# Kernel optimization log

Measured on AMD Instinct MI355X. Metric: run time of the kernel, lower is better.

## Reference

```python
import jax, jax.numpy as jnp
import numpy as np

NUM_CLASSES = 2
CONF_THRESH = 0.05
NMS_THRESH = 0.3
NMS_TOP_K = 5000
TOP_K = 750
VAR0, VAR1 = 0.1, 0.2
NEG = -1e9  # sentinel for suppressed / below-threshold scores

NUM = 16
PRIORS = 131072


def setup_inputs() -> dict:
    key = jax.random.key(0)
    k1, k2, k3 = jax.random.split(key, 3)
    loc_data = jax.random.normal(k1, (NUM, PRIORS, 4), dtype=jnp.float32)
    conf_data = jax.random.uniform(k2, (NUM * PRIORS, NUM_CLASSES), dtype=jnp.float32)
    prior_data = jax.random.uniform(k3, (PRIORS, 4), dtype=jnp.float32)
    return {"loc_data": loc_data, "conf_data": conf_data, "prior_data": prior_data}


def decode(loc, priors):
    # loc, priors: [N, 4] (cx, cy, w, h priors); SSD box decode -> (x1, y1, x2, y2)
    xy = priors[:, :2] + loc[:, :2] * VAR0 * priors[:, 2:]
    wh = priors[:, 2:] * jnp.exp(loc[:, 2:] * VAR1)
    return jnp.concatenate([xy - wh * 0.5, xy + wh * 0.5], axis=-1)


def _area(b):
    return (b[..., 2] - b[..., 0]) * (b[..., 3] - b[..., 1])


def iou_one_to_many(box, boxes):
    # box: [4], boxes: [K, 4]
    lt = jnp.maximum(box[:2], boxes[:, :2])
    rb = jnp.minimum(box[2:], boxes[:, 2:])
    wh = jnp.clip(rb - lt, 0.0)
    inter = wh[:, 0] * wh[:, 1]
    union = _area(box) + _area(boxes) - inter
    return inter / jnp.maximum(union, 1e-12)


def nms_single(boxes, scores):
    # boxes: [P, 4], scores: [P] (one image, one class) -> [TOP_K, 5] (score, x1, y1, x2, y2)
    s = jnp.where(scores > CONF_THRESH, scores, NEG)
    top_s, top_i = jax.lax.top_k(s, NMS_TOP_K)
    top_b = boxes[top_i]  # [K, 4]
    idx_range = jnp.arange(NMS_TOP_K)

    def step(s_work, _):
        idx = jnp.argmax(s_work)
        sc = s_work[idx]
        valid = sc > NEG * 0.5
        box = top_b[idx]
        ious = iou_one_to_many(box, top_b)
        kill = (ious > NMS_THRESH) | (idx_range == idx)
        s_new = jnp.where(kill, NEG, s_work)
        row = jnp.where(valid, jnp.concatenate([sc[None], box]), jnp.zeros((5,), boxes.dtype))
        return s_new, row

    _, rows = jax.lax.scan(step, top_s, None, length=TOP_K)
    return rows  # [TOP_K, 5]


def reference(loc_data, conf_data, prior_data):
    num, P, _ = loc_data.shape
    conf = conf_data.reshape(num, P, NUM_CLASSES).transpose(0, 2, 1)  # [num, C, P]
    batch_priors = jnp.broadcast_to(prior_data, (num, P, 4)).reshape(-1, 4)
    boxes = decode(loc_data.reshape(-1, 4), batch_priors).reshape(num, P, 4)
    # NMS over non-background classes, vmapped over batch and class
    per_image = jax.vmap(nms_single, in_axes=(None, 0))          # over classes
    det = jax.vmap(per_image)(boxes, conf[:, 1:, :])             # [num, C-1, TOP_K, 5]
    bg = jnp.zeros((num, 1, TOP_K, 5), det.dtype)
    return jnp.concatenate([bg, det], axis=1)                     # [num, C, TOP_K, 5]
```

## Files before the change

### kernel.cpp

```cpp
#include <hip/hip_runtime.h>
#include <cmath>

#pragma clang fp contract(off)

typedef unsigned long long ull;

#define NPRIORS 131072
#define NIMG 16
#define KSEL 5000
#define TOPK 750
#define SORTN 8192
#define MW 80
#define NCHUNK 79
#define KSELP (NCHUNK * 64)
#define NBIN 65536

#define MID03 0.30000002682209014892578125

#define WS_PAIRS 0
#define WS_NDIAG 0
#define WS_MCNT 1048576
#define WS_BOXES 1048832
#define WS_SCORES 2328832
#define WS_MASK 2649088
#define WS_HIST (WS_MASK)
#define WS_CNT  (WS_MASK + 4194304)
#define WS_POS  (WS_MASK + 8388608)
#define WS_DIAG (WS_MASK + (size_t)NIMG * KSEL * MW * 8)

__device__ inline ull readlane64(ull t, int l) {
  unsigned lo = (unsigned)__builtin_amdgcn_readlane((int)(unsigned)t, l);
  unsigned hi = (unsigned)__builtin_amdgcn_readlane((int)(unsigned)(t >> 32), l);
  return ((ull)hi << 32) | lo;
}

__device__ inline void softBarrier() {
  asm volatile("s_waitcnt lgkmcnt(0)\n\ts_barrier" ::: "memory");
}

__global__ __launch_bounds__(256) void hist_kernel(const float* __restrict__ conf,
                                                   unsigned int* __restrict__ hist) {
  const int img = blockIdx.y;
  const float4* c4 = (const float4*)conf + (size_t)img * (NPRIORS / 2);
  unsigned int* H = hist + (size_t)img * NBIN;
  for (int q = blockIdx.x * 256 + threadIdx.x; q < NPRIORS / 2; q += 64 * 256) {
    float4 v = c4[q];
    if (v.y > 0.05f) atomicAdd(&H[(__float_as_uint(v.y) >> 12) & 0xFFFFu], 1u);
    if (v.w > 0.05f) atomicAdd(&H[(__float_as_uint(v.w) >> 12) & 0xFFFFu], 1u);
  }
}

__global__ __launch_bounds__(1024) void cutoff_kernel(const unsigned int* __restrict__ hist,
                                                      unsigned int* __restrict__ pos,
                                                      int* __restrict__ meta,
                                                      float4* __restrict__ sboxes,
                                                      float* __restrict__ sscores) {
  const int img = blockIdx.x;
  const int tid = threadIdx.x;
  const int lane = tid & 63;
  const int wv = tid >> 6;
  const unsigned int* H = hist + (size_t)img * NBIN;
  unsigned int* P = pos + (size_t)img * NBIN;
  __shared__ unsigned int csum[1024];
  __shared__ unsigned int suf[1024];
  __shared__ int s_cc;
  __shared__ unsigned int s_cut, s_mc;

  for (int g = 0; g < 64; ++g) {
    unsigned int v = H[g * 1024 + tid];
    for (int m = 1; m < 64; m <<= 1) v += __shfl_xor(v, m);
    if (lane == 0) csum[g * 16 + wv] = v;
  }
  __syncthreads();
  suf[tid] = csum[tid];
  if (tid == 0) s_cc = 0;
  __syncthreads();
  for (int off = 1; off < 1024; off <<= 1) {
    unsigned int v = (tid + off < 1024) ? suf[tid + off] : 0u;
    __syncthreads();
    suf[tid] += v;
    __syncthreads();
  }
  if (suf[tid] >= KSEL && (suf[tid] - csum[tid]) < KSEL) s_cc = tid;
  __syncthreads();
  const int cc = s_cc;
  if (tid == 0) { s_cut = (unsigned int)(cc * 64); s_mc = suf[0]; }
  __syncthreads();
  for (int b = cc * 64 + tid; b < NBIN; b += 1024) {
    int q = b >> 6;
    unsigned int acc = (q + 1 < 1024) ? suf[q + 1] : 0u;
    for (int b2 = b + 1; b2 < (q + 1) * 64; ++b2) acc += H[b2];
    P[b] = acc;
    unsigned int h = H[b];
    if (acc < KSEL && acc + h >= KSEL) { s_cut = (unsigned int)b; s_mc = acc + h; }
  }
  __syncthreads();
  if (tid == 0) {
    meta[img] = (int)min(s_mc, (unsigned int)SORTN);
    meta[16 + img] = (int)s_cut;
  }
  for (int i = tid; i < KSEL; i += 1024) {
    sboxes[(size_t)img * KSEL + i] = make_float4(0.f, 0.f, 0.f, 0.f);
    sscores[(size_t)img * KSEL + i] = -1e9f;
  }
}

__global__ __launch_bounds__(256) void scatter_kernel(const float* __restrict__ conf,
                                                      const unsigned int* __restrict__ pos,
                                                      unsigned int* __restrict__ cnt,
                                                      const int* __restrict__ meta,
                                                      ull* __restrict__ pairs) {
  const int img = blockIdx.y;
  const float4* c4 = (const float4*)conf + (size_t)img * (NPRIORS / 2);
  const unsigned int* P = pos + (size_t)img * NBIN;
  unsigned int* Cn = cnt + (size_t)img * NBIN;
  ull* mypairs = pairs + (size_t)img * SORTN;
  const unsigned int cutval = ((unsigned int)meta[16 + img]) << 12;
  for (int q = blockIdx.x * 256 + threadIdx.x; q < NPRIORS / 2; q += 64 * 256) {
    float4 v = c4[q];
#pragma unroll
    for (int h = 0; h < 2; ++h) {
      float sc = h ? v.w : v.y;
      unsigned int p = 2 * (unsigned int)q + h;
      if (sc > 0.05f) {
        unsigned int u = __float_as_uint(sc);
        if (u >= cutval) {
          unsigned int bin = (u >> 12) & 0xFFFFu;
          unsigned int slot = atomicAdd(&Cn[bin], 1u);
          unsigned int idx = P[bin] + slot;
          if (idx < SORTN)
            mypairs[idx] = ((ull)u << 32) | (ull)(0xFFFFFFFFu - p);
        }
      }
    }
  }
}

__global__ __launch_bounds__(256) void rank_decode_kernel(const ull* __restrict__ pairs,
                                                          const unsigned int* __restrict__ hist,
                                                          const unsigned int* __restrict__ pos,
                                                          const int* __restrict__ meta,
                                                          const float* __restrict__ loc,
                                                          const float* __restrict__ prior,
                                                          float4* __restrict__ sboxes,
                                                          float* __restrict__ sscores) {
#pragma clang fp contract(off)
  const int img = blockIdx.y;
  const int s = blockIdx.x * 256 + threadIdx.x;
  const int mc = meta[img];
  if (s >= mc) return;
  const ull* mypairs = pairs + (size_t)img * SORTN;
  const ull key = mypairs[s];
  const unsigned int u = (unsigned int)(key >> 32);
  const unsigned int bin = (u >> 12) & 0xFFFFu;
  const unsigned int base = pos[(size_t)img * NBIN + bin];
  const unsigned int cb = hist[(size_t)img * NBIN + bin];
  const int end = min((int)(base + cb), mc);
  int rank = 0;
  for (int j = (int)base; j < end; ++j) rank += (mypairs[j] > key);
  const int fp = (int)base + rank;
  if (fp >= KSEL) return;
  const unsigned int p = 0xFFFFFFFFu - (unsigned int)(key & 0xFFFFFFFFu);
  const float* lp = loc + ((size_t)img * NPRIORS + p) * 4;
  const float* pp = prior + (size_t)p * 4;
  float l0 = lp[0], l1 = lp[1], l2 = lp[2], l3 = lp[3];
  float px = pp[0], py = pp[1], pw = pp[2], ph = pp[3];
  float cx = px + (l0 * 0.1f) * pw;
  float cy = py + (l1 * 0.1f) * ph;
  float w = pw * (float)exp((double)(l2 * 0.2f));
  float hh = ph * (float)exp((double)(l3 * 0.2f));
  float4 box;
  box.x = cx - w * 0.5f;
  box.y = cy - hh * 0.5f;
  box.z = cx + w * 0.5f;
  box.w = cy + hh * 0.5f;
  sboxes[(size_t)img * KSEL + fp] = box;
  sscores[(size_t)img * KSEL + fp] = __uint_as_float(u);
}

__global__ __launch_bounds__(256) void mask_build_kernel(const float4* __restrict__ sboxes,
                                                         ull* __restrict__ mask,
                                                         ull* __restrict__ diag,
                                                         ull* __restrict__ ndiag) {
#pragma clang fp contract(off)
  const int jt = blockIdx.x;
  const int sp = blockIdx.y;
  const int img = blockIdx.z;
  if (jt < (sp >> 1)) return;
  const int tid = threadIdx.x;
  const int lane = tid & 63;
  const int wave = tid >> 6;
  __shared__ float4 ib[128];
  const float4* bb = sboxes + (size_t)img * KSEL;
  if (tid < 128) {
    int i = sp * 128 + tid;
    ib[tid] = (i < KSEL) ? bb[i] : make_float4(0.f, 0.f, 0.f, 0.f);
  }
  __syncthreads();
  float4 cb[4];
  float ca[4];
#pragma unroll
  for (int s = 0; s < 4; ++s) {
    int j = jt * 256 + s * 64 + lane;
    cb[s] = (j < KSEL) ? bb[j] : make_float4(0.f, 0.f, 0.f, 0.f);
    ca[s] = (cb[s].z - cb[s].x) * (cb[s].w - cb[s].y);
  }
  ull* mrow = mask + (size_t)img * KSEL * MW;
  ull* dg = diag + (size_t)img * KSELP;
  ull* ndg = ndiag + (size_t)img * KSELP;
  const int grp0 = jt * 4;
  for (int k = 0; k < 32; ++k) {
    const int rr = wave * 32 + k;
    const int strip = 2 * sp + (rr >> 6);
    const int r = rr & 63;
    const int i = sp * 128 + rr;
    const float4 pb = ib[rr];
    const float pa = (pb.z - pb.x) * (pb.w - pb.y);
    ull w[4];
#pragma unroll
    for (int s = 0; s < 4; ++s) {
      float ltx = fmaxf(pb.x, cb[s].x), lty = fmaxf(pb.y, cb[s].y);
      float rbx = fminf(pb.z, cb[s].z), rby = fminf(pb.w, cb[s].w);
      float ww = fmaxf(rbx - ltx, 0.0f), hh = fmaxf(rby - lty, 0.0f);
      float inter = ww * hh;
      float uni = fmaxf(pa + ca[s] - inter, 1e-12f);
      bool cond = ((grp0 + s) != strip) | (lane > r);
      bool kill = cond && ((double)inter > MID03 * (double)uni);
      w[s] = __ballot(kill);
    }
    if (lane == 0 && i < KSEL) {
      ull* wp = mrow + (size_t)i * MW + grp0;
      ((ulonglong2*)wp)[0] = make_ulonglong2(w[0], w[1]);
      ((ulonglong2*)wp)[1] = make_ulonglong2(w[2], w[3]);
#pragma unroll
      for (int s = 0; s < 4; ++s) {
        if (grp0 + s == strip) dg[i] = w[s];
        if (grp0 + s == strip + 1) ndg[i] = w[s];
      }
    }
  }
}

__global__ __launch_bounds__(128) void sweep_kernel(const ull* __restrict__ mask,
                                                    const ull* __restrict__ diag,
                                                    const ull* __restrict__ ndiag,
                                                    const float4* __restrict__ sboxes,
                                                    const float* __restrict__ sscores,
                                                    const int* __restrict__ meta,
                                                    float* __restrict__ out) {
  const int img = blockIdx.x;
  const int tid = threadIdx.x;
  const int lane = tid & 63;
  const bool waveA = (tid < 64);
  const int V = min(meta[img], KSEL);
  const ull* mb = mask + (size_t)img * KSEL * MW;
  const ull* dg = diag + (size_t)img * KSELP;
  const ull* ng = ndiag + (size_t)img * KSELP;
  __shared__ ull mailbox[NCHUNK + 1];
  __shared__ int pickbuf[TOPK];
  __shared__ int s_np[NCHUNK];
  __shared__ int s_start[NCHUNK];
  __shared__ int s_done;
  __shared__ int s_n;
  const int lc = min(lane, 39);

  for (int i = tid; i <= NCHUNK; i += 128) mailbox[i] = 0ULL;
  if (tid == 0) { s_done = 0; s_n = 0; }
  __syncthreads();

  if (V > 0) {
    ull dw = 0, ndw = 0, bridge = 0;
    ull rlo = 0, rhi = 0;
    int nkeep = 0;
    bool adone = false;
    if (waveA) { dw = dg[lane]; ndw = ng[lane]; }

    for (int k = 0; k < NCHUNK; ++k) {
      softBarrier();
      if (s_done) break;
      if (waveA) {
        if (!adone) {
          const int base = k * 64;
          const int nidx = min(base + 64 + lane, KSELP - 1);
          ull dwn = dg[nidx];
          ull ndwn = ng[nidx];
          ull cur = mailbox[k] | bridge;
          bridge = 0ULL;
          const int lim = V - base;
          ull validm = (lim >= 64) ? ~0ULL : ((~0ULL) >> (64 - lim));
          ull avail = (~cur) & validm;
          const int st = nkeep;
          if (lane == 0) s_start[k] = st;
          while (avail != 0ULL && nkeep < TOPK) {
            int r = __builtin_ctzll(avail);
            if (lane == 0) pickbuf[nkeep] = base + r;
            nkeep++;
            ull dr = readlane64(dw, r);
            bridge |= readlane64(ndw, r);
            avail &= ~(dr | (1ULL << r));
          }
          if (lane == 0) s_np[k] = nkeep - st;
          if (nkeep >= TOPK || base + 64 >= V) {
            if (lane == 0) { s_done = 1; s_n = (nkeep < TOPK) ? nkeep : TOPK; }
            adone = true;
          }
          dw = dwn;
          ndw = ndwn;
        }
      } else if (k >= 1) {
        const int np = s_np[k - 1];
        const int st = s_start[k - 1];
        for (int g = 0; g < np; g += 16) {
          ulonglong2 v[16];
#pragma unroll
          for (int q = 0; q < 16; ++q) {
            int t = min(g + q, np - 1);
            int row = pickbuf[st + t];
            v[q] = *(const ulonglong2*)(mb + (size_t)row * MW + 2 * lc);
          }
#pragma unroll
          for (int q = 0; q < 16; ++q) { rlo |= v[q].x; rhi |= v[q].y; }
        }
        const int w = k + 1;
        if (w < NCHUNK) {
          ull t = (w & 1) ? rhi : rlo;
          ull word = readlane64(t, w >> 1);
          if (lane == 0) mailbox[w] = word;
        }
      }
    }
  }

  __syncthreads();
  const int n = s_n;
  float* ob = out + (size_t)img * (2 * TOPK * 5) + TOPK * 5;
  for (int j = tid; j < n; j += 128) {
    int i = pickbuf[j];
    float4 b = sboxes[(size_t)img * KSEL + i];
    float sc = sscores[(size_t)img * KSEL + i];
    float* o = ob + (size_t)j * 5;
    o[0] = sc; o[1] = b.x; o[2] = b.y; o[3] = b.z; o[4] = b.w;
  }
}

extern "C" void kernel_launch(void* const* d_in, const int* in_sizes, int n_in,
                              void* d_out, int out_size, void* d_ws, size_t ws_size,
                              hipStream_t stream) {
  const float* loc = (const float*)d_in[0];
  const float* conf = (const float*)d_in[1];
  const float* prior = (const float*)d_in[2];
  float* out = (float*)d_out;

  char* ws = (char*)d_ws;
  ull* pairs = (ull*)(ws + WS_PAIRS);
  ull* ndiag = (ull*)(ws + WS_NDIAG);
  int* meta = (int*)(ws + WS_MCNT);
  float4* sboxes = (float4*)(ws + WS_BOXES);
  float* sscores = (float*)(ws + WS_SCORES);
  ull* mask = (ull*)(ws + WS_MASK);
  ull* diag = (ull*)(ws + WS_DIAG);
  unsigned int* hist = (unsigned int*)(ws + WS_HIST);
  unsigned int* cnt = (unsigned int*)(ws + WS_CNT);
  unsigned int* pos = (unsigned int*)(ws + WS_POS);

  hipMemsetAsync(d_out, 0, (size_t)out_size * sizeof(float), stream);
  hipMemsetAsync(ws + WS_HIST, 0, 2u * 4194304u, stream);

  {
    dim3 g(64, NIMG);
    hist_kernel<<<g, 256, 0, stream>>>(conf, hist);
  }
  cutoff_kernel<<<NIMG, 1024, 0, stream>>>(hist, pos, meta, sboxes, sscores);
  {
    dim3 g(64, NIMG);
    scatter_kernel<<<g, 256, 0, stream>>>(conf, pos, cnt, meta, pairs);
  }
  {
    dim3 g((SORTN + 255) / 256, NIMG);
    rank_decode_kernel<<<g, 256, 0, stream>>>(pairs, hist, pos, meta, loc, prior, sboxes, sscores);
  }
  {
    dim3 g(20, 40, NIMG);
    mask_build_kernel<<<g, 256, 0, stream>>>(sboxes, mask, diag, ndiag);
  }
  sweep_kernel<<<NIMG, 128, 0, stream>>>(mask, diag, ndiag, sboxes, sscores, meta, out);
}
```

Baseline: 534.5 us.

## Restructure NMS mask build to per-lane row bitmasks with fast IoU test

The IoU mask kernel now gives each lane one row box and loops over 256 column boxes held in shared memory. It assembles 32-bit kill words in registers instead of using one ballot per row per column group, which removes the per-row serialized lane-0 stores. The exact double-precision threshold comparison is replaced by a float FMA test with a narrow uncertainty band, falling back to double only when a wave contains a near-tie. The grid changes to 256x256 tiles, which halves the row-tile count and adds more per-thread work and register pressure.

```diff
diff --git a/kernel.cpp b/kernel.cpp
--- a/kernel.cpp
+++ b/kernel.cpp
@@ -4,6 +4,7 @@
 #pragma clang fp contract(off)
 
 typedef unsigned long long ull;
+typedef unsigned int uint;
 
 #define NPRIORS 131072
 #define NIMG 16
@@ -184,60 +185,86 @@
                                                          ull* __restrict__ ndiag) {
 #pragma clang fp contract(off)
   const int jt = blockIdx.x;
-  const int sp = blockIdx.y;
+  const int rt = blockIdx.y;
   const int img = blockIdx.z;
-  if (jt < (sp >> 1)) return;
+  if (jt < rt) return;
   const int tid = threadIdx.x;
   const int lane = tid & 63;
-  const int wave = tid >> 6;
-  __shared__ float4 ib[128];
+  const int wv = __builtin_amdgcn_readfirstlane(tid >> 6);
   const float4* bb = sboxes + (size_t)img * KSEL;
-  if (tid < 128) {
-    int i = sp * 128 + tid;
-    ib[tid] = (i < KSEL) ? bb[i] : make_float4(0.f, 0.f, 0.f, 0.f);
-  }
-  __syncthreads();
-  float4 cb[4];
-  float ca[4];
+
+  __shared__ float4 cbox[256];
+  __shared__ float carea[256];
+  {
+    int j = jt * 256 + tid;
+    float4 c = (j < KSEL) ? bb[j] : make_float4(0.f, 0.f, 0.f, 0.f);
+    cbox[tid] = c;
+    carea[tid] = (c.z - c.x) * (c.w - c.y);
+  }
+  __syncthreads();
+
+  const int R = rt * 256 + wv * 64;
+  if (R >= KSEL) return;
+  const int i = R + lane;
+  float4 pb = (i < KSEL) ? bb[i] : make_float4(0.f, 0.f, 0.f, 0.f);
+  const float pa = (pb.z - pb.x) * (pb.w - pb.y);
+
+  auto killbit = [&](int j) -> uint {
+    float4 c = cbox[j];
+    float caa = carea[j];
+    float ltx = fmaxf(pb.x, c.x), lty = fmaxf(pb.y, c.y);
+    float rbx = fminf(pb.z, c.z), rby = fminf(pb.w, c.w);
+    float ww = fmaxf(rbx - ltx, 0.0f), hh = fmaxf(rby - lty, 0.0f);
+    float inter = ww * hh;
+    float uni = fmaxf(pa + caa - inter, 1e-12f);
+    float f = fmaf(-0.3f, uni, inter);
+    float band = uni * 0x1p-20f;
+    bool kill = f > band;
+    if (__builtin_expect(__ballot(fabsf(f) <= band) != 0ULL, 0)) {
+      if (fabsf(f) <= band) kill = (double)inter > MID03 * (double)uni;
+    }
+    return kill ? 1u : 0u;
+  };
+
+  uint wl[4], wh[4];
 #pragma unroll
   for (int s = 0; s < 4; ++s) {
-    int j = jt * 256 + s * 64 + lane;
-    cb[s] = (j < KSEL) ? bb[j] : make_float4(0.f, 0.f, 0.f, 0.f);
-    ca[s] = (cb[s].z - cb[s].x) * (cb[s].w - cb[s].y);
-  }
-  ull* mrow = mask + (size_t)img * KSEL * MW;
-  ull* dg = diag + (size_t)img * KSELP;
-  ull* ndg = ndiag + (size_t)img * KSELP;
-  const int grp0 = jt * 4;
-  for (int k = 0; k < 32; ++k) {
-    const int rr = wave * 32 + k;
-    const int strip = 2 * sp + (rr >> 6);
-    const int r = rr & 63;
-    const int i = sp * 128 + rr;
-    const float4 pb = ib[rr];
-    const float pa = (pb.z - pb.x) * (pb.w - pb.y);
-    ull w[4];
-#pragma unroll
-    for (int s = 0; s < 4; ++s) {
-      float ltx = fmaxf(pb.x, cb[s].x), lty = fmaxf(pb.y, cb[s].y);
-      float rbx = fminf(pb.z, cb[s].z), rby = fminf(pb.w, cb[s].w);
-      float ww = fmaxf(rbx - ltx, 0.0f), hh = fmaxf(rby - lty, 0.0f);
-      float inter = ww * hh;
-      float uni = fmaxf(pa + ca[s] - inter, 1e-12f);
-      bool cond = ((grp0 + s) != strip) | (lane > r);
-      bool kill = cond && ((double)inter > MID03 * (double)uni);
-      w[s] = __ballot(kill);
-    }
-    if (lane == 0 && i < KSEL) {
-      ull* wp = mrow + (size_t)i * MW + grp0;
-      ((ulonglong2*)wp)[0] = make_ulonglong2(w[0], w[1]);
-      ((ulonglong2*)wp)[1] = make_ulonglong2(w[2], w[3]);
-#pragma unroll
-      for (int s = 0; s < 4; ++s) {
-        if (grp0 + s == strip) dg[i] = w[s];
-        if (grp0 + s == strip + 1) ndg[i] = w[s];
+    if (jt == rt && s < wv) { wl[s] = 0u; wh[s] = 0u; continue; }
+    uint alo = 0, ahi = 0;
+#pragma unroll 8
+    for (int b = 0; b < 32; ++b) alo |= killbit(s * 64 + b) << b;
+#pragma unroll 8
+    for (int b = 0; b < 32; ++b) ahi |= killbit(s * 64 + 32 + b) << b;
+    wl[s] = alo; wh[s] = ahi;
+  }
+
+  if (jt == rt) {
+    uint mlo, mhi;
+    if (lane < 32) { mlo = 0xFFFFFFFEu << lane; mhi = 0xFFFFFFFFu; }
+    else           { mlo = 0u; mhi = 0xFFFFFFFEu << (lane - 32); }
+    uint dl, dh;
+    if (wv == 0)      { wl[0] &= mlo; wh[0] &= mhi; dl = wl[0]; dh = wh[0]; }
+    else if (wv == 1) { wl[1] &= mlo; wh[1] &= mhi; dl = wl[1]; dh = wh[1]; }
+    else if (wv == 2) { wl[2] &= mlo; wh[2] &= mhi; dl = wl[2]; dh = wh[2]; }
+    else              { wl[3] &= mlo; wh[3] &= mhi; dl = wl[3]; dh = wh[3]; }
+    if (i < KSEL) {
+      diag[(size_t)img * KSELP + i] = ((ull)dh << 32) | dl;
+      if (wv < 3) {
+        uint nl, nh;
+        if (wv == 0)      { nl = wl[1]; nh = wh[1]; }
+        else if (wv == 1) { nl = wl[2]; nh = wh[2]; }
+        else              { nl = wl[3]; nh = wh[3]; }
+        ndiag[(size_t)img * KSELP + i] = ((ull)nh << 32) | nl;
       }
     }
+  }
+  if (jt == rt + 1 && wv == 3 && i < KSEL)
+    ndiag[(size_t)img * KSELP + i] = ((ull)wh[0] << 32) | wl[0];
+
+  if (i < KSEL) {
+    uint* wp = (uint*)(mask + (size_t)img * KSEL * MW + (size_t)i * MW) + jt * 8;
+    *(uint4*)wp = make_uint4(wl[0], wh[0], wl[1], wh[1]);
+    *((uint4*)wp + 1) = make_uint4(wl[2], wh[2], wl[3], wh[3]);
   }
 }
 
@@ -380,7 +407,7 @@
     rank_decode_kernel<<<g, 256, 0, stream>>>(pairs, hist, pos, meta, loc, prior, sboxes, sscores);
   }
   {
-    dim3 g(20, 40, NIMG);
+    dim3 g(20, 20, NIMG);
     mask_build_kernel<<<g, 256, 0, stream>>>(sboxes, mask, diag, ndiag);
   }
   sweep_kernel<<<NIMG, 128, 0, stream>>>(mask, diag, ndiag, sboxes, sscores, meta, out);
```

Measured after the change: 531.2 us. About the same (-0.6%).
